# Performance work log

Measured on AMD Instinct MI355X. Metric: run time of the kernel, lower is better.

Reference implementation:

```python
import jax, jax.numpy as jnp
import numpy as np

N = 100000      # nodes (PF candidates)
E = 1600000     # edges, avg degree 16
CONT = 6        # continuous features
H = 32          # hidden_dim
PDGS = [1, 2, 11, 13, 22, 130, 211]


def _p(k, shape):
    return jax.random.normal(k, shape, jnp.float32) * 0.1


def setup_inputs() -> dict:
    key = jax.random.key(0)
    ks = jax.random.split(key, 24)
    x_cont = jax.random.normal(ks[0], (N, CONT), jnp.float32)
    pdg = jnp.array(PDGS, jnp.int32)[jax.random.randint(ks[1], (N,), 0, 7)]
    sign = jax.random.randint(ks[2], (N,), 0, 2) * 2 - 1
    charge = jax.random.randint(ks[3], (N,), -1, 2)
    pv = jax.random.randint(ks[4], (N,), 0, 8)
    x_cat = jnp.stack([pdg * sign, charge, pv], axis=1).astype(jnp.int32)
    edge_index = jax.random.randint(ks[5], (2, E), 0, N, jnp.int32)
    batch = jnp.zeros((N,), jnp.int32)
    return {
        "x_cont": x_cont, "x_cat": x_cat, "edge_index": edge_index, "batch": batch,
        "W_cont": _p(ks[6], (CONT, H // 2)), "b_cont": jnp.zeros((H // 2,), jnp.float32),
        "T_chrg": _p(ks[7], (3, H // 4)), "T_pdg": _p(ks[8], (7, H // 4)), "T_pv": _p(ks[9], (8, H // 4)),
        "W_cat": _p(ks[10], (3 * H // 4, H // 2)), "b_cat": jnp.zeros((H // 2,), jnp.float32),
        "W_enc": _p(ks[11], (H, H)), "b_enc": jnp.zeros((H,), jnp.float32),
        "g_all": jnp.ones((H,), jnp.float32), "be_all": jnp.zeros((H,), jnp.float32),
        "W_msg": _p(ks[12], (2 * H, H)), "b_msg": jnp.zeros((H,), jnp.float32),
        "g_conv": jnp.ones((H,), jnp.float32), "be_conv": jnp.zeros((H,), jnp.float32),
        "W_out1": _p(ks[13], (H, H // 2)), "b_out1": jnp.zeros((H // 2,), jnp.float32),
        "W_out2": _p(ks[14], (H // 2, 1)), "b_out2": jnp.zeros((1,), jnp.float32),
    }


def _batchnorm(x, gamma, beta, eps=1e-5):
    # training-mode BatchNorm1d: biased batch stats over the node axis
    mu = jnp.mean(x, axis=0)
    var = jnp.mean(jnp.square(x - mu), axis=0)
    return (x - mu) * jax.lax.rsqrt(var + eps) * gamma + beta


def reference(x_cont, x_cat, edge_index, batch,
              W_cont, b_cont, T_chrg, T_pdg, T_pv, W_cat, b_cat,
              W_enc, b_enc, g_all, be_all, W_msg, b_msg, g_conv, be_conv,
              W_out1, b_out1, W_out2, b_out2):
    elu = jax.nn.elu
    emb_cont = elu(x_cont @ W_cont + b_cont)                      # [N, H/2]
    emb_chrg = T_chrg[x_cat[:, 1] + 1]                            # [N, H/4]
    emb_pv = T_pv[x_cat[:, 2]]                                    # [N, H/4]
    pdg_remap = jnp.abs(x_cat[:, 0])
    for i, pdgval in enumerate(PDGS):  # fixed small constant loop, as in original
        pdg_remap = jnp.where(pdg_remap == pdgval, jnp.int32(i), pdg_remap)
    emb_pdg = T_pdg[pdg_remap]                                    # [N, H/4]
    emb_cat = elu(jnp.concatenate([emb_chrg, emb_pdg, emb_pv], axis=1) @ W_cat + b_cat)
    emb = elu(jnp.concatenate([emb_cat, emb_cont], axis=1) @ W_enc + b_enc)
    emb = _batchnorm(emb, g_all, be_all)                          # [N, H]
    # EdgeConv: m_ij = nn([x_i, x_j - x_i]), aggregate by max over incoming edges
    src, dst = edge_index[0], edge_index[1]
    x_i = emb[dst]
    x_j = emb[src]
    msg = jnp.concatenate([x_i, x_j - x_i], axis=1) @ W_msg + b_msg   # [E, H]
    agg = jax.ops.segment_max(msg, dst, num_segments=N)
    agg = jnp.where(jnp.isfinite(agg), agg, 0.0)                  # nodes w/o in-edges -> 0
    emb = emb + _batchnorm(agg, g_conv, be_conv)
    out = elu(emb @ W_out1 + b_out1) @ W_out2 + b_out2            # [N, 1]
    return out.squeeze(-1)
```

## Files before the change

kernel.cpp:

```cpp
#include <hip/hip_runtime.h>
#include <hip/hip_bf16.h>

#define NN 100000
#define EE 1600000
#define NB_SCAN 391

#define NBUCK 782
#define CPAD  16
#define NPART 391
#define NE4   400000
#define CAP   4096
#define CAPSH 12
#define BCAP  2560

typedef __hip_bfloat16 bf16_t;
typedef int int4v __attribute__((ext_vector_type(4)));
typedef float f4 __attribute__((ext_vector_type(4)));

#define PARB  600000
#define EMB   604480
#define PBUF  3804480
#define QBUF  7004480
#define ABUF  10204480
#define SOFF  13404480
#define CURS  (SOFF + 256)
#define ROWP2 (CURS + 12512)
#define OFLB  (ROWP2 + 200000)
#define PEB   (OFLB + 3200004)
#define SRCB  (PEB + 3203072)

#define O_WCONT 0
#define O_BCONT 96
#define O_TCHRG 112
#define O_TPDG  136
#define O_TPV   192
#define O_WCAT  256
#define O_BCAT  640
#define O_WENC  656
#define O_BENC  1680
#define O_GALL  1712
#define O_BEALL 1744
#define O_WMSG  1776
#define O_BMSG  3824
#define O_GCONV 3856
#define O_BECONV 3888
#define O_WOUT1 3920
#define O_BOUT1 4432
#define O_WOUT2 4448
#define O_BOUT2 4464
#define NPAR    4465

__device__ __forceinline__ float bf(unsigned short u) {
    return __uint_as_float(((unsigned)u) << 16);
}
__device__ __forceinline__ f4 elu4(f4 v) {
    f4 r;
    r.x = v.x > 0.0f ? v.x : expm1f(v.x);
    r.y = v.y > 0.0f ? v.y : expm1f(v.y);
    r.z = v.z > 0.0f ? v.z : expm1f(v.z);
    r.w = v.w > 0.0f ? v.w : expm1f(v.w);
    return r;
}
__device__ __forceinline__ f4 f4max(f4 a, f4 b) {
    f4 r;
    r.x = fmaxf(a.x, b.x); r.y = fmaxf(a.y, b.y);
    r.z = fmaxf(a.z, b.z); r.w = fmaxf(a.w, b.w);
    return r;
}

struct InitArgs {
    const void* p[19];
    const unsigned short* wdet;
    int*        flagw;
    float*      par;
    int*        curs;
    float*      stats;
    int*        ofl;
    int*        tcur;
};

__global__ __launch_bounds__(256) void k_init(InitArgs a)
{
    const int offs[20] = {O_WCONT,O_BCONT,O_TCHRG,O_TPDG,O_TPV,O_WCAT,O_BCAT,O_WENC,
                          O_BENC,O_GALL,O_BEALL,O_WMSG,O_BMSG,O_GCONV,O_BECONV,
                          O_WOUT1,O_BOUT1,O_WOUT2,O_BOUT2,NPAR};
    __shared__ int sflag;
    int b = blockIdx.x, tid = threadIdx.x;
    int g = b * 256 + tid;
    if (g < NBUCK) a.curs[g * CPAD] = g << CAPSH;
    if (g < 128) a.stats[g] = 0.0f;
    if (g == 0) { a.ofl[0] = 0; *a.tcur = NBUCK << CAPSH; }
    if (b == 0) {
        if (tid == 0) sflag = 0;
        __syncthreads();
        int bad = 0;
        for (int i = tid; i < 1024; i += 256) {
            unsigned e = (a.wdet[i] >> 7) & 0xFFu;
            if (e >= 137u) bad = 1;
        }
        if (bad) atomicOr(&sflag, 1);
        __syncthreads();
        int f32 = sflag;
        if (tid == 0) *a.flagw = f32;
        for (int i = tid; i < NPAR; i += 256) {
            int t = 0;
            while (offs[t + 1] <= i) t++;
            int l = i - offs[t];
            const void* s = a.p[t];
            a.par[i] = f32 ? ((const float*)s)[l] : bf(((const unsigned short*)s)[l]);
        }
    }
}

struct SMemPart {
    int cnt[NBUCK];
    int lstart[NBUCK];
    int gstart[NBUCK];
    int tsum[256];
    unsigned short bkof[4096];
    int staged[4096];
};
struct SMemEmb  { float wc[96], bc[16], tc[24], tp[56], tv[64],
                  wcat[384], bcat[16], we[1024], be[32], ls[64]; };
union SMemA { SMemPart p; SMemEmb e; };

__global__ __launch_bounds__(256, 1) void k_fA(
    const int* __restrict__ eidx, int* __restrict__ curs,
    int* __restrict__ pe, int* __restrict__ ofl, int2* __restrict__ ofl2,
    const void* __restrict__ xc, const int* __restrict__ x_cat,
    const float* __restrict__ par, const int* __restrict__ flag,
    float* __restrict__ emb, float* __restrict__ stats)
{
    __shared__ alignas(16) SMemA sm;
    int tid = threadIdx.x;
    int b = blockIdx.x;

    if (b < NPART) {
        for (int i = tid; i < NBUCK; i += 256) sm.p.cnt[i] = 0;
        __syncthreads();
        const int4v* src4 = (const int4v*)eidx;
        const int4v* dst4 = (const int4v*)(eidx + EE);
        int i0 = b << 10;
        int i1 = i0 + 1024; if (i1 > NE4) i1 = NE4;
        int nE = (i1 - i0) * 4;
        for (int i = i0 + tid; i < i1; i += 256) {
            int4v d = dst4[i];
            atomicAdd(&sm.p.cnt[d.x >> 7], 1);
            atomicAdd(&sm.p.cnt[d.y >> 7], 1);
            atomicAdd(&sm.p.cnt[d.z >> 7], 1);
            atomicAdd(&sm.p.cnt[d.w >> 7], 1);
        }
        __syncthreads();
        int base = tid * 4;
        int c0 = (base     < NBUCK) ? sm.p.cnt[base    ] : 0;
        int c1 = (base + 1 < NBUCK) ? sm.p.cnt[base + 1] : 0;
        int c2 = (base + 2 < NBUCK) ? sm.p.cnt[base + 2] : 0;
        int c3 = (base + 3 < NBUCK) ? sm.p.cnt[base + 3] : 0;
        int s = c0 + c1 + c2 + c3;
        sm.p.tsum[tid] = s;
        __syncthreads();
        for (int off = 1; off < 256; off <<= 1) {
            int x = (tid >= off) ? sm.p.tsum[tid - off] : 0;
            __syncthreads();
            sm.p.tsum[tid] += x;
            __syncthreads();
        }
        int run = sm.p.tsum[tid] - s;
        if (base < NBUCK) {
            sm.p.lstart[base] = run;
            if (c0) sm.p.gstart[base] = atomicAdd(&curs[base * CPAD], c0);
            run += c0;
        }
        if (base + 1 < NBUCK) {
            sm.p.lstart[base + 1] = run;
            if (c1) sm.p.gstart[base + 1] = atomicAdd(&curs[(base + 1) * CPAD], c1);
            run += c1;
        }
        if (base + 2 < NBUCK) {
            sm.p.lstart[base + 2] = run;
            if (c2) sm.p.gstart[base + 2] = atomicAdd(&curs[(base + 2) * CPAD], c2);
            run += c2;
        }
        if (base + 3 < NBUCK) {
            sm.p.lstart[base + 3] = run;
            if (c3) sm.p.gstart[base + 3] = atomicAdd(&curs[(base + 3) * CPAD], c3);
            run += c3;
        }
        __syncthreads();
        for (int i = tid; i < NBUCK; i += 256) {
            int st = sm.p.lstart[i], c = sm.p.cnt[i];
            for (int j = 0; j < c; j++) sm.p.bkof[st + j] = (unsigned short)i;
        }
        __syncthreads();
        for (int i = tid; i < NBUCK; i += 256) sm.p.cnt[i] = 0;
        __syncthreads();
        for (int i = i0 + tid; i < i1; i += 256) {
            int4v s4 = src4[i];
            int4v d4 = dst4[i];
            #define PLACE(SS, DD) { \
                int bk = (DD) >> 7; \
                int r = atomicAdd(&sm.p.cnt[bk], 1); \
                sm.p.staged[sm.p.lstart[bk] + r] = ((SS) << 7) | ((DD) & 127); }
            PLACE(s4.x, d4.x) PLACE(s4.y, d4.y) PLACE(s4.z, d4.z) PLACE(s4.w, d4.w)
            #undef PLACE
        }
        __syncthreads();
        for (int j = tid; j < nE; j += 256) {
            int bk = sm.p.bkof[j];
            int slot = sm.p.gstart[bk] + (j - sm.p.lstart[bk]);
            int packed = sm.p.staged[j];
            if (slot < ((bk + 1) << CAPSH)) pe[slot] = packed;
            else { int oi = atomicAdd(ofl, 1); ofl2[oi] = make_int2(bk, packed); }
        }
        return;
    }

    {
        float* s;
        s=sm.e.wc;   for(int i=tid;i<96;  i+=256) s[i]=par[O_WCONT+i];
        s=sm.e.bc;   for(int i=tid;i<16;  i+=256) s[i]=par[O_BCONT+i];
        s=sm.e.tc;   for(int i=tid;i<24;  i+=256) s[i]=par[O_TCHRG+i];
        s=sm.e.tp;   for(int i=tid;i<56;  i+=256) s[i]=par[O_TPDG+i];
        s=sm.e.tv;   for(int i=tid;i<64;  i+=256) s[i]=par[O_TPV+i];
        s=sm.e.wcat; for(int i=tid;i<384; i+=256) s[i]=par[O_WCAT+i];
        s=sm.e.bcat; for(int i=tid;i<16;  i+=256) s[i]=par[O_BCAT+i];
        s=sm.e.we;   for(int i=tid;i<1024;i+=256) s[i]=par[O_WENC+i];
        s=sm.e.be;   for(int i=tid;i<32;  i+=256) s[i]=par[O_BENC+i];
        if (tid < 64) sm.e.ls[tid] = 0.0f;
    }
    __syncthreads();

    int n = (b - NPART) * 256 + tid;
    float v[64];
    #pragma unroll
    for (int i = 0; i < 64; i++) v[i] = 0.0f;

    if (n < NN) {
        f4* sWc4 = (f4*)sm.e.wc;  f4* sbc4 = (f4*)sm.e.bc;
        f4* sTc4 = (f4*)sm.e.tc;  f4* sTp4 = (f4*)sm.e.tp;  f4* sTv4 = (f4*)sm.e.tv;
        f4* sWcat4 = (f4*)sm.e.wcat; f4* sbcat4 = (f4*)sm.e.bcat;
        f4* sWe4 = (f4*)sm.e.we;  f4* sbe4 = (f4*)sm.e.be;

        float x0,x1,x2,x3,x4,x5;
        if (*flag) {
            const float* xr = (const float*)xc + (size_t)n * 6;
            x0=xr[0]; x1=xr[1]; x2=xr[2]; x3=xr[3]; x4=xr[4]; x5=xr[5];
        } else {
            const unsigned* xr = (const unsigned*)xc + (size_t)n * 3;
            unsigned w0=xr[0], w1=xr[1], w2=xr[2];
            x0=__uint_as_float(w0<<16); x1=__uint_as_float(w0 & 0xFFFF0000u);
            x2=__uint_as_float(w1<<16); x3=__uint_as_float(w1 & 0xFFFF0000u);
            x4=__uint_as_float(w2<<16); x5=__uint_as_float(w2 & 0xFFFF0000u);
        }

        f4 ec[4];
        #pragma unroll
        for (int g = 0; g < 4; g++) {
            f4 acc = sbc4[g];
            acc += x0 * sWc4[0*4+g]; acc += x1 * sWc4[1*4+g]; acc += x2 * sWc4[2*4+g];
            acc += x3 * sWc4[3*4+g]; acc += x4 * sWc4[4*4+g]; acc += x5 * sWc4[5*4+g];
            ec[g] = elu4(acc);
        }

        int c0 = x_cat[n*3+0], c1 = x_cat[n*3+1], c2 = x_cat[n*3+2];
        int a0 = c0 < 0 ? -c0 : c0;
        int pi = (a0==1)?0:(a0==2)?1:(a0==11)?2:(a0==13)?3:(a0==22)?4:(a0==130)?5:6;
        int ci = c1 + 1;

        f4 t0a = sTc4[ci*2],  t0b = sTc4[ci*2+1];
        f4 t1a = sTp4[pi*2],  t1b = sTp4[pi*2+1];
        f4 t2a = sTv4[c2*2],  t2b = sTv4[c2*2+1];

        f4 ecat[4];
        #pragma unroll
        for (int g = 0; g < 4; g++) {
            f4 acc = sbcat4[g];
            #pragma unroll
            for (int k = 0; k < 4; k++) acc += t0a[k] * sWcat4[(k     )*4+g];
            #pragma unroll
            for (int k = 0; k < 4; k++) acc += t0b[k] * sWcat4[(4 + k )*4+g];
            #pragma unroll
            for (int k = 0; k < 4; k++) acc += t1a[k] * sWcat4[(8 + k )*4+g];
            #pragma unroll
            for (int k = 0; k < 4; k++) acc += t1b[k] * sWcat4[(12 + k)*4+g];
            #pragma unroll
            for (int k = 0; k < 4; k++) acc += t2a[k] * sWcat4[(16 + k)*4+g];
            #pragma unroll
            for (int k = 0; k < 4; k++) acc += t2b[k] * sWcat4[(20 + k)*4+g];
            ecat[g] = elu4(acc);
        }

        f4* o = (f4*)(emb + (size_t)n * 32);
        #pragma unroll
        for (int cg = 0; cg < 8; cg++) {
            f4 acc = sbe4[cg];
            #pragma unroll
            for (int kg = 0; kg < 4; kg++) {
                #pragma unroll
                for (int k = 0; k < 4; k++)
                    acc += ecat[kg][k] * sWe4[(kg*4+k)*8 + cg];
            }
            #pragma unroll
            for (int kg = 0; kg < 4; kg++) {
                #pragma unroll
                for (int k = 0; k < 4; k++)
                    acc += ec[kg][k] * sWe4[(16 + kg*4+k)*8 + cg];
            }
            f4 val = elu4(acc);
            o[cg] = val;
            #pragma unroll
            for (int k = 0; k < 4; k++) {
                v[cg*4+k]      = val[k];
                v[32+cg*4+k]   = val[k] * val[k];
            }
        }
    }

    int lane = tid & 63;
    #pragma unroll
    for (int st = 0; st < 6; st++) {
        int off = 1 << st;
        int keep = (lane >> st) & 1;
        int L2 = 32 >> st;
        #pragma unroll
        for (int i = 0; i < 32; i++) {
            if (i < L2) {
                float lo = v[i], hi = v[L2 + i];
                float sent = keep ? lo : hi;
                float got = __shfl_xor(sent, off);
                v[i] = (keep ? hi : lo) + got;
            }
        }
    }
    int idx = ((lane&1)<<5)|((lane&2)<<3)|((lane&4)<<1)|((lane&8)>>1)|((lane&16)>>3)|((lane&32)>>5);
    atomicAdd(&sm.e.ls[idx], v[0]);
    __syncthreads();
    if (tid < 64) atomicAdd(&stats[tid], sm.e.ls[tid]);
}

struct SMemCsr { int stage[BCAP]; int cnt[128]; int sc[128]; int ex[128]; int tl; };
struct SMemPq  { float wp[1024], wq[1024], bp[32], bq[32], ssc[32], ssh[32]; };
union SMemB { SMemCsr c; SMemPq q; };

__global__ __launch_bounds__(256) void k_fB(
    const int* __restrict__ curs, const int* __restrict__ pe,
    const int* __restrict__ ofl, const int2* __restrict__ ofl2,
    int* __restrict__ tcur, int2* __restrict__ rowp2, int* __restrict__ srcl,
    const float* __restrict__ emb, const float* __restrict__ stats,
    const float* __restrict__ par, float* __restrict__ P, float* __restrict__ Q)
{
    __shared__ alignas(16) SMemB sm;
    int tid = threadIdx.x;
    int b = blockIdx.x;

    if (b < NBUCK) {
        int beg = b << CAPSH;
        int m_res = curs[b * CPAD] - beg;
        int stored = m_res < CAP ? m_res : CAP;
        int no = ofl[0];
        if (tid < 128) sm.c.cnt[tid] = 0;
        __syncthreads();
        for (int i = tid; i < stored; i += 256) {
            int p = pe[beg + i];
            if (i < BCAP) sm.c.stage[i] = p;
            atomicAdd(&sm.c.cnt[p & 127], 1);
        }
        for (int j = tid; j < no; j += 256) {
            int2 oe = ofl2[j];
            if (oe.x == b) atomicAdd(&sm.c.cnt[oe.y & 127], 1);
        }
        __syncthreads();
        if (tid < 128) sm.c.sc[tid] = sm.c.cnt[tid];
        __syncthreads();
        for (int off = 1; off < 128; off <<= 1) {
            int x = (tid >= off && tid < 128) ? sm.c.sc[tid - off] : 0;
            __syncthreads();
            if (tid < 128) sm.c.sc[tid] += x;
            __syncthreads();
        }
        int obeg = beg;
        if (m_res > CAP) {
            if (tid == 0) sm.c.tl = atomicAdd(tcur, m_res);
            __syncthreads();
            obeg = sm.c.tl;
        }
        if (tid < 128) {
            int e0 = sm.c.sc[tid] - sm.c.cnt[tid];
            int deg = sm.c.cnt[tid];
            sm.c.ex[tid] = e0;
            int node = b * 128 + tid;
            if (node < NN) rowp2[node] = make_int2(obeg + e0, obeg + e0 + deg);
            sm.c.cnt[tid] = 0;
        }
        __syncthreads();
        for (int i = tid; i < stored; i += 256) {
            int p = (i < BCAP) ? sm.c.stage[i] : pe[beg + i];
            int dl = p & 127;
            int r = atomicAdd(&sm.c.cnt[dl], 1);
            srcl[obeg + sm.c.ex[dl] + r] = p >> 7;
        }
        for (int j = tid; j < no; j += 256) {
            int2 oe = ofl2[j];
            if (oe.x == b) {
                int dl = oe.y & 127;
                int r = atomicAdd(&sm.c.cnt[dl], 1);
                srcl[obeg + sm.c.ex[dl] + r] = oe.y >> 7;
            }
        }
        return;
    }

    if (tid < 32) {
        float mu  = stats[tid] * (1.0f / NN);
        float var = stats[32 + tid] * (1.0f / NN) - mu * mu;
        float s   = par[O_GALL + tid] * rsqrtf(var + 1e-5f);
        sm.q.ssc[tid] = s;
        sm.q.ssh[tid] = par[O_BEALL + tid] - mu * s;
    }
    __syncthreads();
    for (int e = tid; e < 1024; e += 256) {
        int k = e >> 5;
        float w1 = par[O_WMSG + e];
        float w2 = par[O_WMSG + 1024 + e];
        sm.q.wp[e] = sm.q.ssc[k] * (w1 - w2);
        sm.q.wq[e] = sm.q.ssc[k] * w2;
    }
    if (tid < 32) {
        float aP = par[O_BMSG + tid], aQ = 0.0f;
        for (int k = 0; k < 32; k++) {
            float w1 = par[O_WMSG + k*32 + tid];
            float w2 = par[O_WMSG + (k+32)*32 + tid];
            aP += sm.q.ssh[k] * (w1 - w2);
            aQ += sm.q.ssh[k] * w2;
        }
        sm.q.bp[tid] = aP;
        sm.q.bq[tid] = aQ;
    }
    __syncthreads();

    int n = (b - NBUCK) * 256 + tid;
    if (n >= NN) return;

    f4* sWP4 = (f4*)sm.q.wp; f4* sWQ4 = (f4*)sm.q.wq;
    f4* sbP4 = (f4*)sm.q.bp; f4* sbQ4 = (f4*)sm.q.bq;
    const f4* er = (const f4*)(emb + (size_t)n * 32);
    f4 e[8];
    #pragma unroll
    for (int g = 0; g < 8; g++) e[g] = er[g];
    f4* pr = (f4*)(P + (size_t)n * 32);
    f4* qr = (f4*)(Q + (size_t)n * 32);
    #pragma unroll
    for (int cg = 0; cg < 8; cg++) {
        f4 aP = sbP4[cg];
        f4 aQ = sbQ4[cg];
        #pragma unroll
        for (int kg = 0; kg < 8; kg++) {
            #pragma unroll
            for (int k = 0; k < 4; k++) {
                float ek = e[kg][k];
                aP += ek * sWP4[(kg*4+k)*8 + cg];
                aQ += ek * sWQ4[(kg*4+k)*8 + cg];
            }
        }
        pr[cg] = aP;
        qr[cg] = aQ;
    }
}

__global__ __launch_bounds__(256) void k_gather(
    const int2* __restrict__ rowp2, const int* __restrict__ srcl,
    const float* __restrict__ Q, const float* __restrict__ P,
    float* __restrict__ agg)
{
    int tid = threadIdx.x;
    int lane = tid & 63;
    int wave = tid >> 6;
    int half  = lane >> 5;
    int hl    = lane & 31;
    int slice = hl >> 3;
    int cg    = hl & 7;
    int n = (blockIdx.x * 4 + wave) * 2 + half;
    int2 be = rowp2[n];
    int beg = be.x, end = be.y;
    const f4* Q4 = (const f4*)Q;

    f4 pv = (f4){0.f, 0.f, 0.f, 0.f};
    if (hl < 8 && end > beg) pv = ((const f4*)P)[(size_t)n * 8 + hl];

    f4 m = {-INFINITY, -INFINITY, -INFINITY, -INFINITY};
    for (int e = beg + slice; e < end; e += 16) {
        int e1 = min(e + 4,  end - 1);
        int e2 = min(e + 8,  end - 1);
        int e3 = min(e + 12, end - 1);
        int s0 = __builtin_nontemporal_load(&srcl[e]);
        int s1 = __builtin_nontemporal_load(&srcl[e1]);
        int s2 = __builtin_nontemporal_load(&srcl[e2]);
        int s3 = __builtin_nontemporal_load(&srcl[e3]);
        f4 q0 = Q4[(size_t)s0 * 8 + cg];
        f4 q1 = Q4[(size_t)s1 * 8 + cg];
        f4 q2 = Q4[(size_t)s2 * 8 + cg];
        f4 q3 = Q4[(size_t)s3 * 8 + cg];
        q0 = f4max(q0, q1);
        q2 = f4max(q2, q3);
        m = f4max(m, f4max(q0, q2));
    }
    #pragma unroll
    for (int off = 8; off < 32; off <<= 1) {
        m.x = fmaxf(m.x, __shfl_xor(m.x, off));
        m.y = fmaxf(m.y, __shfl_xor(m.y, off));
        m.z = fmaxf(m.z, __shfl_xor(m.z, off));
        m.w = fmaxf(m.w, __shfl_xor(m.w, off));
    }
    if (hl < 8) {
        f4 o;
        if (end > beg) o = m + pv;
        else           o = (f4){0.f, 0.f, 0.f, 0.f};
        ((f4*)agg)[(size_t)n * 8 + hl] = o;
    }
}

__global__ __launch_bounds__(256) void k_stats(const float* __restrict__ xin,
                                               float* __restrict__ outsums, int count)
{
    __shared__ float ls[64];
    int tid = threadIdx.x;
    if (tid < 64) ls[tid] = 0.0f;
    __syncthreads();
    int idx = blockIdx.x * 256 + tid;
    int stride = gridDim.x * 256;
    int c = idx & 31;
    float s = 0.0f, q = 0.0f;
    for (int i = idx; i < count; i += stride) {
        float v = xin[i];
        s += v; q += v * v;
    }
    s += __shfl_xor(s, 32);
    q += __shfl_xor(q, 32);
    if ((tid & 63) < 32) {
        atomicAdd(&ls[c], s);
        atomicAdd(&ls[32 + c], q);
    }
    __syncthreads();
    if (tid < 64) atomicAdd(&outsums[tid], ls[tid]);
}

__global__ __launch_bounds__(256, 1) void k_out(
    const float* __restrict__ emb, const float* __restrict__ agg,
    const float* __restrict__ par, const float* __restrict__ stats,
    const int* __restrict__ flag, void* __restrict__ out)
{
    __shared__ f4 sW14[128];
    __shared__ f4 sb14[4], sW24[4];
    __shared__ f4 sc14[8], sh14[8], sc24[8], sh24[8];
    __shared__ float sb2s;
    int tid = threadIdx.x;
    {
        float* s = (float*)sW14;
        for (int i = tid; i < 512; i += 256) s[i] = par[O_WOUT1 + i];
    }
    if (tid < 16) {
        ((float*)sb14)[tid] = par[O_BOUT1 + tid];
        ((float*)sW24)[tid] = par[O_WOUT2 + tid];
    }
    if (tid < 32) {
        float mu  = stats[tid] * (1.0f / NN);
        float var = stats[32 + tid] * (1.0f / NN) - mu * mu;
        float s   = par[O_GALL + tid] * rsqrtf(var + 1e-5f);
        ((float*)sc14)[tid] = s;
        ((float*)sh14)[tid] = par[O_BEALL + tid] - mu * s;
        float mu2  = stats[64 + tid] * (1.0f / NN);
        float var2 = stats[96 + tid] * (1.0f / NN) - mu2 * mu2;
        float s2   = par[O_GCONV + tid] * rsqrtf(var2 + 1e-5f);
        ((float*)sc24)[tid] = s2;
        ((float*)sh24)[tid] = par[O_BECONV + tid] - mu2 * s2;
    }
    if (tid == 0) sb2s = par[O_BOUT2];
    __syncthreads();

    int n = blockIdx.x * 256 + tid;
    if (n >= NN) return;

    const f4* er = (const f4*)(emb + (size_t)n * 32);
    const f4* ar = (const f4*)(agg + (size_t)n * 32);
    f4 h[8];
    #pragma unroll
    for (int g = 0; g < 8; g++) {
        f4 ev = er[g];
        f4 av = ar[g];
        h[g] = ev * sc14[g] + sh14[g] + av * sc24[g] + sh24[g];
    }
    f4 o1[4];
    #pragma unroll
    for (int g = 0; g < 4; g++) {
        f4 acc = sb14[g];
        #pragma unroll
        for (int kg = 0; kg < 8; kg++) {
            #pragma unroll
            for (int k = 0; k < 4; k++)
                acc += h[kg][k] * sW14[(kg*4+k)*4 + g];
        }
        o1[g] = elu4(acc);
    }
    float acc = sb2s;
    #pragma unroll
    for (int g = 0; g < 4; g++) {
        f4 p = o1[g] * sW24[g];
        acc += p.x + p.y + p.z + p.w;
    }

    if (*flag) ((float*)out)[n] = acc;
    else       ((bf16_t*)out)[n] = __float2bfloat16(acc);
}


extern "C" void kernel_launch(void* const* d_in, const int* in_sizes, int n_in,
                              void* d_out, int out_size, void* d_ws, size_t ws_size,
                              hipStream_t stream)
{
    const void* x_cont = d_in[0];
    const int* x_cat = (const int*)d_in[1];
    const int* eidx  = (const int*)d_in[2];

    float* ws    = (float*)d_ws;
    float* par   = ws + PARB;
    float* emb   = ws + EMB;
    float* P     = ws + PBUF;
    float* Q     = ws + QBUF;
    float* agg   = ws + ABUF;
    float* stats = ws + SOFF;
    int*   flag  = (int*)(stats + 128);
    int*   tcur  = (int*)(stats + 130);
    int*   curs  = (int*)(ws + CURS);
    int2*  rowp2 = (int2*)(ws + ROWP2);
    int*   ofl   = (int*)(ws + OFLB);
    int2*  ofl2  = (int2*)(ws + OFLB + 2);
    int*   pe    = (int*)(ws + PEB);
    int*   srcl  = (int*)(ws + SRCB);

    InitArgs ia;
    for (int t = 0; t < 19; t++) ia.p[t] = d_in[4 + t];
    ia.wdet = (const unsigned short*)d_in[11];
    ia.flagw = flag; ia.par = par; ia.curs = curs; ia.stats = stats;
    ia.ofl = ofl; ia.tcur = tcur;
    k_init<<<16, 256, 0, stream>>>(ia);

    k_fA<<<NPART + NB_SCAN, 256, 0, stream>>>(eidx, curs, pe, ofl, ofl2,
                                              x_cont, x_cat, par, flag, emb, stats);
    k_fB<<<NBUCK + NB_SCAN, 256, 0, stream>>>(curs, pe, ofl, ofl2, tcur, rowp2, srcl,
                                              emb, stats, par, P, Q);
    k_gather<<<NN / 8, 256, 0, stream>>>(rowp2, srcl, Q, P, agg);
    k_stats<<<512, 256, 0, stream>>>(agg, stats + 64, NN * 32);
    k_out<<<NB_SCAN, 256, 0, stream>>>(emb, agg, par, stats, flag, d_out);
}
```

Before: 255.0 us.

## Store Q in bf16 for gather and widen dst buckets to 256 nodes

The per-node Q projection is now stored as packed bf16 instead of fp32, which halves the bytes the edge gather reads for each random source lookup; values are unpacked to fp32 before the max. Separately, the CSR bucketing now uses 256 destination nodes per bucket instead of 128, so there are half as many buckets with twice the capacity and all 256 threads take part in each bucket's scan. The bf16 rounding of Q adds error to the max-aggregated messages, and the larger buckets grow shared memory use and raise per-bucket atomic contention.

```diff
diff --git a/kernel.cpp b/kernel.cpp
--- a/kernel.cpp
+++ b/kernel.cpp
@@ -5,13 +5,13 @@
 #define EE 1600000
 #define NB_SCAN 391
 
-#define NBUCK 782
+#define NBUCK 391
 #define CPAD  16
 #define NPART 391
 #define NE4   400000
-#define CAP   4096
-#define CAPSH 12
-#define BCAP  2560
+#define CAP   8192
+#define CAPSH 13
+#define BCAP  4608
 
 typedef __hip_bfloat16 bf16_t;
 typedef int int4v __attribute__((ext_vector_type(4)));
@@ -53,6 +53,10 @@
 __device__ __forceinline__ float bf(unsigned short u) {
     return __uint_as_float(((unsigned)u) << 16);
 }
+__device__ __forceinline__ unsigned short f2b(float f) {
+    __hip_bfloat16 h = __float2bfloat16(f);
+    return *reinterpret_cast<unsigned short*>(&h);
+}
 __device__ __forceinline__ f4 elu4(f4 v) {
     f4 r;
     r.x = v.x > 0.0f ? v.x : expm1f(v.x);
@@ -65,6 +69,14 @@
     f4 r;
     r.x = fmaxf(a.x, b.x); r.y = fmaxf(a.y, b.y);
     r.z = fmaxf(a.z, b.z); r.w = fmaxf(a.w, b.w);
+    return r;
+}
+__device__ __forceinline__ f4 unpack_q(uint2 q) {
+    f4 r;
+    r.x = __uint_as_float(q.x << 16);
+    r.y = __uint_as_float(q.x & 0xFFFF0000u);
+    r.z = __uint_as_float(q.y << 16);
+    r.w = __uint_as_float(q.y & 0xFFFF0000u);
     return r;
 }
 
@@ -145,10 +157,10 @@
         int nE = (i1 - i0) * 4;
         for (int i = i0 + tid; i < i1; i += 256) {
             int4v d = dst4[i];
-            atomicAdd(&sm.p.cnt[d.x >> 7], 1);
-            atomicAdd(&sm.p.cnt[d.y >> 7], 1);
-            atomicAdd(&sm.p.cnt[d.z >> 7], 1);
-            atomicAdd(&sm.p.cnt[d.w >> 7], 1);
+            atomicAdd(&sm.p.cnt[d.x >> 8], 1);
+            atomicAdd(&sm.p.cnt[d.y >> 8], 1);
+            atomicAdd(&sm.p.cnt[d.z >> 8], 1);
+            atomicAdd(&sm.p.cnt[d.w >> 8], 1);
         }
         __syncthreads();
         int base = tid * 4;
@@ -198,9 +210,9 @@
             int4v s4 = src4[i];
             int4v d4 = dst4[i];
             #define PLACE(SS, DD) { \
-                int bk = (DD) >> 7; \
+                int bk = (DD) >> 8; \
                 int r = atomicAdd(&sm.p.cnt[bk], 1); \
-                sm.p.staged[sm.p.lstart[bk] + r] = ((SS) << 7) | ((DD) & 127); }
+                sm.p.staged[sm.p.lstart[bk] + r] = ((SS) << 8) | ((DD) & 255); }
             PLACE(s4.x, d4.x) PLACE(s4.y, d4.y) PLACE(s4.z, d4.z) PLACE(s4.w, d4.w)
             #undef PLACE
         }
@@ -338,7 +350,7 @@
     if (tid < 64) atomicAdd(&stats[tid], sm.e.ls[tid]);
 }
 
-struct SMemCsr { int stage[BCAP]; int cnt[128]; int sc[128]; int ex[128]; int tl; };
+struct SMemCsr { int stage[BCAP]; int cnt[256]; int sc[256]; int ex[256]; int tl; };
 struct SMemPq  { float wp[1024], wq[1024], bp[32], bq[32], ssc[32], ssh[32]; };
 union SMemB { SMemCsr c; SMemPq q; };
 
@@ -347,7 +359,8 @@
     const int* __restrict__ ofl, const int2* __restrict__ ofl2,
     int* __restrict__ tcur, int2* __restrict__ rowp2, int* __restrict__ srcl,
     const float* __restrict__ emb, const float* __restrict__ stats,
-    const float* __restrict__ par, float* __restrict__ P, float* __restrict__ Q)
+    const float* __restrict__ par, float* __restrict__ P,
+    unsigned short* __restrict__ Qh)
 {
     __shared__ alignas(16) SMemB sm;
     int tid = threadIdx.x;
@@ -358,24 +371,24 @@
         int m_res = curs[b * CPAD] - beg;
         int stored = m_res < CAP ? m_res : CAP;
         int no = ofl[0];
-        if (tid < 128) sm.c.cnt[tid] = 0;
+        sm.c.cnt[tid] = 0;
         __syncthreads();
         for (int i = tid; i < stored; i += 256) {
             int p = pe[beg + i];
             if (i < BCAP) sm.c.stage[i] = p;
-            atomicAdd(&sm.c.cnt[p & 127], 1);
+            atomicAdd(&sm.c.cnt[p & 255], 1);
         }
         for (int j = tid; j < no; j += 256) {
             int2 oe = ofl2[j];
-            if (oe.x == b) atomicAdd(&sm.c.cnt[oe.y & 127], 1);
-        }
-        __syncthreads();
-        if (tid < 128) sm.c.sc[tid] = sm.c.cnt[tid];
-        __syncthreads();
-        for (int off = 1; off < 128; off <<= 1) {
-            int x = (tid >= off && tid < 128) ? sm.c.sc[tid - off] : 0;
+            if (oe.x == b) atomicAdd(&sm.c.cnt[oe.y & 255], 1);
+        }
+        __syncthreads();
+        sm.c.sc[tid] = sm.c.cnt[tid];
+        __syncthreads();
+        for (int off = 1; off < 256; off <<= 1) {
+            int x = (tid >= off) ? sm.c.sc[tid - off] : 0;
             __syncthreads();
-            if (tid < 128) sm.c.sc[tid] += x;
+            sm.c.sc[tid] += x;
             __syncthreads();
         }
         int obeg = beg;
@@ -384,27 +397,27 @@
             __syncthreads();
             obeg = sm.c.tl;
         }
-        if (tid < 128) {
+        {
             int e0 = sm.c.sc[tid] - sm.c.cnt[tid];
             int deg = sm.c.cnt[tid];
             sm.c.ex[tid] = e0;
-            int node = b * 128 + tid;
+            int node = b * 256 + tid;
             if (node < NN) rowp2[node] = make_int2(obeg + e0, obeg + e0 + deg);
             sm.c.cnt[tid] = 0;
         }
         __syncthreads();
         for (int i = tid; i < stored; i += 256) {
             int p = (i < BCAP) ? sm.c.stage[i] : pe[beg + i];
-            int dl = p & 127;
+            int dl = p & 255;
             int r = atomicAdd(&sm.c.cnt[dl], 1);
-            srcl[obeg + sm.c.ex[dl] + r] = p >> 7;
+            srcl[obeg + sm.c.ex[dl] + r] = p >> 8;
         }
         for (int j = tid; j < no; j += 256) {
             int2 oe = ofl2[j];
             if (oe.x == b) {
-                int dl = oe.y & 127;
+                int dl = oe.y & 255;
                 int r = atomicAdd(&sm.c.cnt[dl], 1);
-                srcl[obeg + sm.c.ex[dl] + r] = oe.y >> 7;
+                srcl[obeg + sm.c.ex[dl] + r] = oe.y >> 8;
             }
         }
         return;
@@ -448,7 +461,7 @@
     #pragma unroll
     for (int g = 0; g < 8; g++) e[g] = er[g];
     f4* pr = (f4*)(P + (size_t)n * 32);
-    f4* qr = (f4*)(Q + (size_t)n * 32);
+    uint2* qr = (uint2*)(Qh + (size_t)n * 32);
     #pragma unroll
     for (int cg = 0; cg < 8; cg++) {
         f4 aP = sbP4[cg];
@@ -463,13 +476,16 @@
             }
         }
         pr[cg] = aP;
-        qr[cg] = aQ;
+        uint2 qp;
+        qp.x = (unsigned)f2b(aQ.x) | ((unsigned)f2b(aQ.y) << 16);
+        qp.y = (unsigned)f2b(aQ.z) | ((unsigned)f2b(aQ.w) << 16);
+        qr[cg] = qp;
     }
 }
 
 __global__ __launch_bounds__(256) void k_gather(
     const int2* __restrict__ rowp2, const int* __restrict__ srcl,
-    const float* __restrict__ Q, const float* __restrict__ P,
+    const unsigned short* __restrict__ Qh, const float* __restrict__ P,
     float* __restrict__ agg)
 {
     int tid = threadIdx.x;
@@ -482,7 +498,7 @@
     int n = (blockIdx.x * 4 + wave) * 2 + half;
     int2 be = rowp2[n];
     int beg = be.x, end = be.y;
-    const f4* Q4 = (const f4*)Q;
+    const uint2* Q2 = (const uint2*)Qh;
 
     f4 pv = (f4){0.f, 0.f, 0.f, 0.f};
     if (hl < 8 && end > beg) pv = ((const f4*)P)[(size_t)n * 8 + hl];
@@ -496,10 +512,10 @@
         int s1 = __builtin_nontemporal_load(&srcl[e1]);
         int s2 = __builtin_nontemporal_load(&srcl[e2]);
         int s3 = __builtin_nontemporal_load(&srcl[e3]);
-        f4 q0 = Q4[(size_t)s0 * 8 + cg];
-        f4 q1 = Q4[(size_t)s1 * 8 + cg];
-        f4 q2 = Q4[(size_t)s2 * 8 + cg];
-        f4 q3 = Q4[(size_t)s3 * 8 + cg];
+        f4 q0 = unpack_q(Q2[(size_t)s0 * 8 + cg]);
+        f4 q1 = unpack_q(Q2[(size_t)s1 * 8 + cg]);
+        f4 q2 = unpack_q(Q2[(size_t)s2 * 8 + cg]);
+        f4 q3 = unpack_q(Q2[(size_t)s3 * 8 + cg]);
         q0 = f4max(q0, q1);
         q2 = f4max(q2, q3);
         m = f4max(m, f4max(q0, q2));
@@ -625,7 +641,7 @@
     float* par   = ws + PARB;
     float* emb   = ws + EMB;
     float* P     = ws + PBUF;
-    float* Q     = ws + QBUF;
+    unsigned short* Qh = (unsigned short*)(ws + QBUF);
     float* agg   = ws + ABUF;
     float* stats = ws + SOFF;
     int*   flag  = (int*)(stats + 128);
@@ -647,8 +663,8 @@
     k_fA<<<NPART + NB_SCAN, 256, 0, stream>>>(eidx, curs, pe, ofl, ofl2,
                                               x_cont, x_cat, par, flag, emb, stats);
     k_fB<<<NBUCK + NB_SCAN, 256, 0, stream>>>(curs, pe, ofl, ofl2, tcur, rowp2, srcl,
-                                              emb, stats, par, P, Q);
-    k_gather<<<NN / 8, 256, 0, stream>>>(rowp2, srcl, Q, P, agg);
+                                              emb, stats, par, P, Qh);
+    k_gather<<<NN / 8, 256, 0, stream>>>(rowp2, srcl, Qh, P, agg);
     k_stats<<<512, 256, 0, stream>>>(agg, stats + 64, NN * 32);
     k_out<<<NB_SCAN, 256, 0, stream>>>(emb, agg, par, stats, flag, d_out);
 }
```

New measurement: 245.2 us. 1.04x faster.
